# Kernel optimization log

Hardware: AMD Instinct MI355X
Metric: run time of the kernel (lower is better)

## Reference

```python
import jax, jax.numpy as jnp
import numpy as np

N, M, W, F_IN, REP, HYP = 4096, 33, 7, 256, 128, 128
BN_EPS = 1e-5


def setup_inputs() -> dict:
    key = jax.random.key(0)
    ks = iter(jax.random.split(key, 40))
    rn = lambda *s: jax.random.normal(next(ks), s, dtype=jnp.float32) * 0.05
    inp = {
        'X': jax.random.normal(next(ks), (N, M, W, F_IN), dtype=jnp.float32),
        'Y': jax.random.uniform(next(ks), (N, M), dtype=jnp.float32),
        'C': jax.random.uniform(next(ks), (N, M, W), dtype=jnp.float32),
        # message_p.linear
        'msg_W': rn(REP, F_IN), 'msg_b': rn(REP),
        # 2-layer GRU (batch_first) inside message_p
        'gru0_Wih': rn(3 * REP, REP), 'gru0_Whh': rn(3 * REP, REP),
        'gru0_bih': rn(3 * REP), 'gru0_bhh': rn(3 * REP),
        'gru1_Wih': rn(3 * REP, REP), 'gru1_Whh': rn(3 * REP, REP),
        'gru1_bih': rn(3 * REP), 'gru1_bhh': rn(3 * REP),
        # Nei_p.linear (target features -> rep)
        'lin_W': rn(REP, F_IN), 'lin_b': rn(REP),
        # Nei_p.linear2 (2*rep -> rep)
        'lin2_W': rn(REP, 2 * REP), 'lin2_b': rn(REP),
        # GRUCell
        'cell_Wih': rn(3 * REP, REP), 'cell_Whh': rn(3 * REP, REP),
        'cell_bih': rn(3 * REP), 'cell_bhh': rn(3 * REP),
        # hypothesis head
        'hyp_W': rn(HYP, REP), 'hyp_b': rn(HYP),
        'bn_gamma': jnp.ones((HYP,), jnp.float32), 'bn_beta': jnp.zeros((HYP,), jnp.float32),
        'bn_mean': jnp.zeros((HYP,), jnp.float32), 'bn_var': jnp.ones((HYP,), jnp.float32),
        'out_W': rn(1, HYP), 'out_b': rn(1),
    }
    return inp


def _gru_gates(x_gates, h, Whh, bhh):
    # PyTorch GRU/GRUCell math. x_gates = x @ Wih^T + bih, shape [n, 3r]
    hg = h @ Whh.T + bhh
    xr, xz, xn = jnp.split(x_gates, 3, axis=-1)
    hr, hz, hn = jnp.split(hg, 3, axis=-1)
    r = jax.nn.sigmoid(xr + hr)
    z = jax.nn.sigmoid(xz + hz)
    n = jnp.tanh(xn + r * hn)
    return (1.0 - z) * n + z * h


def _gru_layer(x, Wih, Whh, bih, bhh):
    # x: [n, w, d] -> [n, w, r]; scan over time
    xg = jnp.einsum('nwd,gd->nwg', x, Wih) + bih  # [n, w, 3r]
    h0 = jnp.zeros((x.shape[0], Whh.shape[1]), x.dtype)

    def step(h, xg_t):
        h2 = _gru_gates(xg_t, h, Whh, bhh)
        return h2, h2

    _, ys = jax.lax.scan(step, h0, jnp.swapaxes(xg, 0, 1))
    return jnp.swapaxes(ys, 0, 1)


def _forward(X, Y, C, msg_W, msg_b, gru0_Wih, gru0_Whh, gru0_bih, gru0_bhh,
             gru1_Wih, gru1_Whh, gru1_bih, gru1_bhh, lin_W, lin_b, lin2_W, lin2_b,
             cell_Wih, cell_Whh, cell_bih, cell_bhh, hyp_W, hyp_b,
             bn_gamma, bn_beta, bn_mean, bn_var, out_W, out_b):
    target_X = X[:, 0]          # [n, w, f]
    target_Y = Y[:, 0]          # [n]
    neighbor_X = X[:, 1:]       # [n, m-1, w, f]
    neighbor_P = C[:, 1:]       # [n, m-1, w]

    # message_p: linear then weighted sum over neighbors (broadcast-mul-sum)
    h = jnp.einsum('nmwf,rf->nmwr', neighbor_X, msg_W) + msg_b      # [n, m-1, w, r]
    h = jnp.einsum('nmwr,nmw->nwr', h, neighbor_P)                   # [n, w, r]
    h = _gru_layer(h, gru0_Wih, gru0_Whh, gru0_bih, gru0_bhh)
    h_nei = _gru_layer(h, gru1_Wih, gru1_Whh, gru1_bih, gru1_bhh)    # [n, w, r]

    h_self = jnp.einsum('nwf,rf->nwr', target_X, lin_W) + lin_b      # [n, w, r]

    # 7-step cat -> linear2 -> tanh -> GRUCell loop (hx starts at zeros)
    hx0 = jnp.zeros((X.shape[0], lin2_W.shape[0]), X.dtype)

    def step(hx, inputs):
        hn_t, hs_t = inputs
        hx = jnp.tanh(jnp.concatenate((hx, hn_t), axis=-1) @ lin2_W.T + lin2_b)
        xg = hs_t @ cell_Wih.T + cell_bih
        hx = _gru_gates(xg, hx, cell_Whh, cell_bhh)
        return hx, None

    hx, _ = jax.lax.scan(step, hx0, (jnp.swapaxes(h_nei, 0, 1), jnp.swapaxes(h_self, 0, 1)))

    # head: linear -> BN (eval, running stats) -> relu -> linear (dropout = identity)
    h0 = hx @ hyp_W.T + hyp_b
    h0 = (h0 - bn_mean) * jax.lax.rsqrt(bn_var + BN_EPS) * bn_gamma + bn_beta
    h0 = jax.nn.relu(h0)
    y = (h0 @ out_W.T + out_b).reshape(-1)                           # logits [n]

    # binary_cross_entropy_with_logits, mean reduction
    loss = jnp.mean(jnp.maximum(y, 0.0) - y * target_Y + jnp.log1p(jnp.exp(-jnp.abs(y))))
    return loss, jax.nn.sigmoid(y)


def reference(X, Y, C, msg_W, msg_b, gru0_Wih, gru0_Whh, gru0_bih, gru0_bhh,
              gru1_Wih, gru1_Whh, gru1_bih, gru1_bhh, lin_W, lin_b, lin2_W, lin2_b,
              cell_Wih, cell_Whh, cell_bih, cell_bhh, hyp_W, hyp_b,
              bn_gamma, bn_beta, bn_mean, bn_var, out_W, out_b):
    return _forward(X, Y, C, msg_W, msg_b, gru0_Wih, gru0_Whh, gru0_bih, gru0_bhh,
                    gru1_Wih, gru1_Whh, gru1_bih, gru1_bhh, lin_W, lin_b, lin2_W, lin2_b,
                    cell_Wih, cell_Whh, cell_bih, cell_bhh, hyp_W, hyp_b,
                    bn_gamma, bn_beta, bn_mean, bn_var, out_W, out_b)
```

## Files before the change

kernel.cpp:

```cpp
#include <hip/hip_runtime.h>
#include <math.h>

#define N_    4096
#define NPAIR (N_ * 7)

typedef unsigned short u16;
typedef __attribute__((ext_vector_type(8))) short bf16x8;
typedef __attribute__((ext_vector_type(4))) float f32x4;

__device__ __forceinline__ float sigm(float x) { return 1.0f / (1.0f + __expf(-x)); }
__device__ __forceinline__ float tanh_fast(float x) { return 2.0f / (1.0f + __expf(-2.0f * x)) - 1.0f; }
__device__ __forceinline__ float bf2f(u16 u) { return __uint_as_float(((unsigned)u) << 16); }
__device__ __forceinline__ u16 f2bf(float f) {
  unsigned u = __float_as_uint(f);
  return (u16)((u + 0x7FFFu + ((u >> 16) & 1u)) >> 16);
}
__device__ __forceinline__ f32x4 mfma16(bf16x8 a, bf16x8 b, f32x4 c) {
  return __builtin_amdgcn_mfma_f32_16x16x32_bf16(a, b, c, 0, 0, 0);
}

__global__ __launch_bounds__(256) void k_prep_all(
    const float* __restrict__ msg_W, const float* __restrict__ lin_W,
    const float* __restrict__ g0_Wih, const float* __restrict__ g1_Wih,
    const float* __restrict__ c_Wih, const float* __restrict__ lin2_W,
    const float* __restrict__ g0_Whh, const float* __restrict__ g1_Whh,
    const float* __restrict__ c_Whh, const float* __restrict__ hyp_W,
    u16* __restrict__ wbase)
{
  const int task = blockIdx.y;
  const int i = blockIdx.x * 256 + threadIdx.x;
  int R, KD, stride, koff, doff;
  const float* src;
  switch (task) {
    case 0:  R=128; KD=256; stride=256; koff=0;   src=msg_W;  doff=0;      break;
    case 1:  R=128; KD=256; stride=256; koff=0;   src=lin_W;  doff=32768;  break;
    case 2:  R=384; KD=128; stride=128; koff=0;   src=g0_Wih; doff=65536;  break;
    case 3:  R=384; KD=128; stride=128; koff=0;   src=g1_Wih; doff=114688; break;
    case 4:  R=384; KD=128; stride=128; koff=0;   src=c_Wih;  doff=163840; break;
    case 5:  R=128; KD=128; stride=256; koff=128; src=lin2_W; doff=212992; break;
    case 6:  R=128; KD=128; stride=256; koff=0;   src=lin2_W; doff=229376; break;
    case 7:  R=384; KD=128; stride=128; koff=0;   src=g0_Whh; doff=245760; break;
    case 8:  R=384; KD=128; stride=128; koff=0;   src=g1_Whh; doff=294912; break;
    case 9:  R=384; KD=128; stride=128; koff=0;   src=c_Whh;  doff=344064; break;
    default: R=128; KD=128; stride=128; koff=0;   src=hyp_W;  doff=393216; break;
  }
  if (i >= R * KD) return;
  const int r = i / KD, k = i - r * KD;
  wbase[doff + i] = f2bf(src[(size_t)r * stride + koff + k]);
}

__global__ __launch_bounds__(256) void k1_fused(
    const float* __restrict__ X, const float* __restrict__ C,
    const u16* __restrict__ msgw, const u16* __restrict__ linw,
    const float* __restrict__ msg_b, const float* __restrict__ lin_b,
    u16* __restrict__ hmsg, u16* __restrict__ hself)
{
  __shared__ u16 sXW[16 * 256];
  __shared__ u16 sTX[16 * 256];
  __shared__ float s_ps[16];
  const int tid = threadIdx.x, wave = tid >> 6, lane = tid & 63;
  const int p0 = blockIdx.x * 16;

  for (int q = 0; q < 4; ++q) {
    const int lp = wave * 4 + q;
    const int p = p0 + lp;
    const int n = p / 7, w = p - n * 7;
    const float* xb = X + ((size_t)(n * 33 + 1) * 7 + w) * 256 + lane * 4;
    const float* cb = C + (size_t)(n * 33 + 1) * 7 + w;
    float4 acc = make_float4(0.f, 0.f, 0.f, 0.f);
    float ps = 0.f;
    #pragma unroll 4
    for (int m = 0; m < 32; ++m) {
      const float c = cb[m * 7];
      const float4 x4 = *(const float4*)(xb + (size_t)m * 1792);
      acc.x += c * x4.x; acc.y += c * x4.y; acc.z += c * x4.z; acc.w += c * x4.w;
      ps += c;
    }
    const int sb = lp * 512 + ((lane * 8) ^ ((lp & 7) << 4));
    ushort4 o = {f2bf(acc.x), f2bf(acc.y), f2bf(acc.z), f2bf(acc.w)};
    *(ushort4*)((char*)sXW + sb) = o;
    const float4 t4 = *(const float4*)(X + ((size_t)(n * 33) * 7 + w) * 256 + lane * 4);
    ushort4 ot = {f2bf(t4.x), f2bf(t4.y), f2bf(t4.z), f2bf(t4.w)};
    *(ushort4*)((char*)sTX + sb) = ot;
    if (lane == 0) s_ps[lp] = ps;
  }
  __syncthreads();

  const int l15 = lane & 15, lq = lane >> 4;
  bf16x8 ax[8], at[8];
  #pragma unroll
  for (int kc = 0; kc < 8; ++kc) {
    const int off = l15 * 512 + ((lq * 16 + kc * 64) ^ ((l15 & 7) << 4));
    ax[kc] = *(const bf16x8*)((const char*)sXW + off);
    at[kc] = *(const bf16x8*)((const char*)sTX + off);
  }
  float psr[4];
  #pragma unroll
  for (int r = 0; r < 4; ++r) psr[r] = s_ps[lq * 4 + r];

  #pragma unroll
  for (int ct = 0; ct < 2; ++ct) {
    const int col = (wave + ct * 4) * 16 + l15;
    f32x4 am = {0.f, 0.f, 0.f, 0.f}, as = {0.f, 0.f, 0.f, 0.f};
    #pragma unroll
    for (int kc = 0; kc < 8; ++kc) {
      const bf16x8 bm = *(const bf16x8*)(msgw + (size_t)col * 256 + lq * 8 + kc * 32);
      const bf16x8 bl = *(const bf16x8*)(linw + (size_t)col * 256 + lq * 8 + kc * 32);
      am = mfma16(ax[kc], bm, am);
      as = mfma16(at[kc], bl, as);
    }
    const float mb = msg_b[col], lb = lin_b[col];
    #pragma unroll
    for (int r = 0; r < 4; ++r) {
      const int p = p0 + lq * 4 + r;
      hmsg[(size_t)p * 128 + col]  = f2bf(am[r] + mb * psr[r]);
      hself[(size_t)p * 128 + col] = f2bf(as[r] + lb);
    }
  }
}

__device__ __forceinline__ void stage16(u16* __restrict__ dst,
                                        const u16* __restrict__ src,
                                        int n0, int tid)
{
  #pragma unroll
  for (int it = 0; it < 7; ++it) {
    const int chunk = it * 256 + tid;
    const int w = chunk >> 8, rem = chunk & 255;
    const int n = rem >> 4, d0 = (rem & 15) * 8;
    const uint4 v = *(const uint4*)(src + ((size_t)(n0 + n) * 7 + w) * 128 + d0);
    *(uint4*)((char*)dst + w * 4096 + n * 256 + ((d0 * 2) ^ ((n & 7) << 4))) = v;
  }
}

__device__ __forceinline__ void gru_stage(
    u16* __restrict__ sin, u16* __restrict__ sout,
    const u16* __restrict__ wih, const u16* __restrict__ whh,
    const float* __restrict__ bih, const float* __restrict__ bhh,
    int wave, int l15, int lq)
{
  bf16x8 wi[6][4], wh[6][4];
  float binit[6], bxn[2];
  #pragma unroll
  for (int i = 0; i < 6; ++i) {
    const int g = (wave + i * 4) * 16 + l15;
    #pragma unroll
    for (int kc = 0; kc < 4; ++kc) {
      wi[i][kc] = *(const bf16x8*)(wih + (size_t)g * 128 + lq * 8 + kc * 32);
      wh[i][kc] = *(const bf16x8*)(whh + (size_t)g * 128 + lq * 8 + kc * 32);
    }
    binit[i] = (i < 4) ? (bih[g] + bhh[g]) : bhh[g];
    if (i >= 4) bxn[i - 4] = bih[g];
  }
  float hold[2][4] = {{0.f, 0.f, 0.f, 0.f}, {0.f, 0.f, 0.f, 0.f}};

  for (int w = 0; w < 7; ++w) {
    bf16x8 afx[4], afh[4];
    #pragma unroll
    for (int kc = 0; kc < 4; ++kc) {
      const int off = l15 * 256 + ((lq * 16 + kc * 64) ^ ((l15 & 7) << 4));
      afx[kc] = *(const bf16x8*)((const char*)sin + w * 4096 + off);
      if (w) afh[kc] = *(const bf16x8*)((const char*)sout + (w - 1) * 4096 + off);
    }
    f32x4 acc[6], accx[2];
    #pragma unroll
    for (int i = 0; i < 6; ++i) acc[i] = (f32x4){binit[i], binit[i], binit[i], binit[i]};
    #pragma unroll
    for (int t = 0; t < 2; ++t) accx[t] = (f32x4){bxn[t], bxn[t], bxn[t], bxn[t]};

    #pragma unroll
    for (int i = 0; i < 6; ++i) {
      #pragma unroll
      for (int kc = 0; kc < 4; ++kc) {
        if (i < 4) acc[i] = mfma16(afx[kc], wi[i][kc], acc[i]);
        else       accx[i - 4] = mfma16(afx[kc], wi[i][kc], accx[i - 4]);
        if (w) acc[i] = mfma16(afh[kc], wh[i][kc], acc[i]);
      }
    }
    #pragma unroll
    for (int t = 0; t < 2; ++t) {
      const int d = (wave + t * 4) * 16 + l15;
      #pragma unroll
      for (int r = 0; r < 4; ++r) {
        const float rg = sigm(acc[t][r]);
        const float zg = sigm(acc[t + 2][r]);
        const float nn = tanh_fast(accx[t][r] + rg * acc[t + 4][r]);
        const float hv = (1.f - zg) * nn + zg * hold[t][r];
        hold[t][r] = hv;
        const int n = lq * 4 + r;
        *(u16*)((char*)sout + w * 4096 + n * 256 + ((d * 2) ^ ((n & 7) << 4))) = f2bf(hv);
      }
    }
    __syncthreads();
  }
}

__global__ __launch_bounds__(256, 1) void k_chain(
    const u16* __restrict__ hmsg, const u16* __restrict__ hself,
    const u16* __restrict__ wbase,
    const float* __restrict__ g0_bih, const float* __restrict__ g0_bhh,
    const float* __restrict__ g1_bih, const float* __restrict__ g1_bhh,
    const float* __restrict__ lin2_b,
    const float* __restrict__ c_bih, const float* __restrict__ c_bhh,
    const float* __restrict__ hyp_b,
    const float* __restrict__ bn_g, const float* __restrict__ bn_be,
    const float* __restrict__ bn_m, const float* __restrict__ bn_v,
    const float* __restrict__ out_W, const float* __restrict__ out_b,
    const float* __restrict__ Y,
    float* __restrict__ outp, float* __restrict__ bloss)
{
  __shared__ u16 sA[7 * 2048];
  __shared__ u16 sB[7 * 2048];
  __shared__ u16 sC[2048];
  __shared__ u16 sD[2048];
  __shared__ float s_red[16][66];
  __shared__ float s_ls[16];

  const int tid = threadIdx.x;
  const int lane = tid & 63, wave = tid >> 6;
  const int l15 = lane & 15, lq = lane >> 4;
  const int n0 = blockIdx.x * 16;

  const u16* g0wih = wbase + 65536;
  const u16* g1wih = wbase + 114688;
  const u16* cwih  = wbase + 163840;
  const u16* l2w   = wbase + 212992;
  const u16* w2a   = wbase + 229376;
  const u16* whh0  = wbase + 245760;
  const u16* whh1  = wbase + 294912;
  const u16* whhc  = wbase + 344064;
  const u16* hypw  = wbase + 393216;

  stage16(sA, hmsg, n0, tid);
  __syncthreads();

  gru_stage(sA, sB, g0wih, whh0, g0_bih, g0_bhh, wave, l15, lq);
  gru_stage(sB, sA, g1wih, whh1, g1_bih, g1_bhh, wave, l15, lq);

  stage16(sB, hself, n0, tid);
  __syncthreads();

  {
    bf16x8 lw[2][4], wa[2][4], wi[6][4], wh[6][4];
    float b2[2], cbin[6], cbxn[2];
    #pragma unroll
    for (int t = 0; t < 2; ++t) {
      const int d = (wave + t * 4) * 16 + l15;
      #pragma unroll
      for (int kc = 0; kc < 4; ++kc) {
        lw[t][kc] = *(const bf16x8*)(l2w + (size_t)d * 128 + lq * 8 + kc * 32);
        wa[t][kc] = *(const bf16x8*)(w2a + (size_t)d * 128 + lq * 8 + kc * 32);
      }
      b2[t] = lin2_b[d];
    }
    #pragma unroll
    for (int i = 0; i < 6; ++i) {
      const int g = (wave + i * 4) * 16 + l15;
      #pragma unroll
      for (int kc = 0; kc < 4; ++kc) {
        wi[i][kc] = *(const bf16x8*)(cwih + (size_t)g * 128 + lq * 8 + kc * 32);
        wh[i][kc] = *(const bf16x8*)(whhc + (size_t)g * 128 + lq * 8 + kc * 32);
      }
      cbin[i] = (i < 4) ? (c_bih[g] + c_bhh[g]) : c_bhh[g];
      if (i >= 4) cbxn[i - 4] = c_bih[g];
    }

    for (int w = 0; w < 7; ++w) {
      bf16x8 af1[4], afx_[4];
      #pragma unroll
      for (int kc = 0; kc < 4; ++kc) {
        const int off = l15 * 256 + ((lq * 16 + kc * 64) ^ ((l15 & 7) << 4));
        af1[kc] = *(const bf16x8*)((const char*)sA + w * 4096 + off);
        if (w) afx_[kc] = *(const bf16x8*)((const char*)sD + off);
      }
      f32x4 a1[2];
      #pragma unroll
      for (int t = 0; t < 2; ++t) a1[t] = (f32x4){b2[t], b2[t], b2[t], b2[t]};
      #pragma unroll
      for (int t = 0; t < 2; ++t)
        #pragma unroll
        for (int kc = 0; kc < 4; ++kc) {
          a1[t] = mfma16(af1[kc], lw[t][kc], a1[t]);
          if (w) a1[t] = mfma16(afx_[kc], wa[t][kc], a1[t]);
        }
      float hx1[2][4];
      #pragma unroll
      for (int t = 0; t < 2; ++t) {
        const int d = (wave + t * 4) * 16 + l15;
        #pragma unroll
        for (int r = 0; r < 4; ++r) {
          hx1[t][r] = tanh_fast(a1[t][r]);
          const int n = lq * 4 + r;
          *(u16*)((char*)sC + n * 256 + ((d * 2) ^ ((n & 7) << 4))) = f2bf(hx1[t][r]);
        }
      }
      __syncthreads();

      bf16x8 afs[4], aft[4];
      #pragma unroll
      for (int kc = 0; kc < 4; ++kc) {
        const int off = l15 * 256 + ((lq * 16 + kc * 64) ^ ((l15 & 7) << 4));
        afs[kc] = *(const bf16x8*)((const char*)sB + w * 4096 + off);
        aft[kc] = *(const bf16x8*)((const char*)sC + off);
      }
      f32x4 acc[6], accx[2];
      #pragma unroll
      for (int i = 0; i < 6; ++i) acc[i] = (f32x4){cbin[i], cbin[i], cbin[i], cbin[i]};
      #pragma unroll
      for (int t = 0; t < 2; ++t) accx[t] = (f32x4){cbxn[t], cbxn[t], cbxn[t], cbxn[t]};
      #pragma unroll
      for (int i = 0; i < 6; ++i)
        #pragma unroll
        for (int kc = 0; kc < 4; ++kc) {
          if (i < 4) acc[i] = mfma16(afs[kc], wi[i][kc], acc[i]);
          else       accx[i - 4] = mfma16(afs[kc], wi[i][kc], accx[i - 4]);
          acc[i] = mfma16(aft[kc], wh[i][kc], acc[i]);
        }
      #pragma unroll
      for (int t = 0; t < 2; ++t) {
        const int d = (wave + t * 4) * 16 + l15;
        #pragma unroll
        for (int r = 0; r < 4; ++r) {
          const float rg = sigm(acc[t][r]);
          const float zg = sigm(acc[t + 2][r]);
          const float nn = tanh_fast(accx[t][r] + rg * acc[t + 4][r]);
          const float hv = (1.f - zg) * nn + zg * hx1[t][r];
          const int n = lq * 4 + r;
          *(u16*)((char*)sD + n * 256 + ((d * 2) ^ ((n & 7) << 4))) = f2bf(hv);
        }
      }
      __syncthreads();
    }
  }

  {
    bf16x8 af[4];
    #pragma unroll
    for (int kc = 0; kc < 4; ++kc) {
      const int off = l15 * 256 + ((lq * 16 + kc * 64) ^ ((l15 & 7) << 4));
      af[kc] = *(const bf16x8*)((const char*)sD + off);
    }
    f32x4 ah[2];
    float sc[2], mu[2], be[2], ow[2];
    #pragma unroll
    for (int t = 0; t < 2; ++t) {
      const int q = (wave + t * 4) * 16 + l15;
      const float hb = hyp_b[q];
      ah[t] = (f32x4){hb, hb, hb, hb};
      sc[t] = rsqrtf(bn_v[q] + 1e-5f) * bn_g[q];
      mu[t] = bn_m[q]; be[t] = bn_be[q]; ow[t] = out_W[q];
      #pragma unroll
      for (int kc = 0; kc < 4; ++kc) {
        const bf16x8 hf = *(const bf16x8*)(hypw + (size_t)q * 128 + lq * 8 + kc * 32);
        ah[t] = mfma16(af[kc], hf, ah[t]);
      }
    }
    float part[4] = {0.f, 0.f, 0.f, 0.f};
    #pragma unroll
    for (int t = 0; t < 2; ++t)
      #pragma unroll
      for (int r = 0; r < 4; ++r) {
        const float v = (ah[t][r] - mu[t]) * sc[t] + be[t];
        part[r] += ow[t] * fmaxf(v, 0.f);
      }
    #pragma unroll
    for (int r = 0; r < 4; ++r) s_red[lq * 4 + r][wave * 16 + l15] = part[r];
  }
  __syncthreads();
  if (tid < 16) {
    const int n = tid;
    float y = out_b[0];
    #pragma unroll 8
    for (int c = 0; c < 64; ++c) y += s_red[n][c];
    outp[1 + n0 + n] = 1.f / (1.f + __expf(-y));
    const float tY = Y[(size_t)(n0 + n) * 33];
    s_ls[n] = fmaxf(y, 0.f) - y * tY + log1pf(__expf(-fabsf(y)));
  }
  __syncthreads();
  if (tid == 0) {
    float s = 0.f;
    #pragma unroll
    for (int j = 0; j < 16; ++j) s += s_ls[j];
    bloss[blockIdx.x] = s;
  }
}

__global__ __launch_bounds__(256) void k3_loss(const float* __restrict__ bloss,
                                               float* __restrict__ out)
{
  __shared__ float s[256];
  s[threadIdx.x] = bloss[threadIdx.x];
  __syncthreads();
  for (int off = 128; off > 0; off >>= 1) {
    if (threadIdx.x < off) s[threadIdx.x] += s[threadIdx.x + off];
    __syncthreads();
  }
  if (threadIdx.x == 0) out[0] = s[0] * (1.0f / 4096.0f);
}

extern "C" void kernel_launch(void* const* d_in, const int* in_sizes, int n_in,
                              void* d_out, int out_size, void* d_ws, size_t ws_size,
                              hipStream_t stream) {
  const float* X       = (const float*)d_in[0];
  const float* Y       = (const float*)d_in[1];
  const float* C       = (const float*)d_in[2];
  const float* msg_W   = (const float*)d_in[3];
  const float* msg_b   = (const float*)d_in[4];
  const float* g0_Wih  = (const float*)d_in[5];
  const float* g0_Whh  = (const float*)d_in[6];
  const float* g0_bih  = (const float*)d_in[7];
  const float* g0_bhh  = (const float*)d_in[8];
  const float* g1_Wih  = (const float*)d_in[9];
  const float* g1_Whh  = (const float*)d_in[10];
  const float* g1_bih  = (const float*)d_in[11];
  const float* g1_bhh  = (const float*)d_in[12];
  const float* lin_W   = (const float*)d_in[13];
  const float* lin_b   = (const float*)d_in[14];
  const float* lin2_W  = (const float*)d_in[15];
  const float* lin2_b  = (const float*)d_in[16];
  const float* c_Wih   = (const float*)d_in[17];
  const float* c_Whh   = (const float*)d_in[18];
  const float* c_bih   = (const float*)d_in[19];
  const float* c_bhh   = (const float*)d_in[20];
  const float* hyp_W   = (const float*)d_in[21];
  const float* hyp_b   = (const float*)d_in[22];
  const float* bn_g    = (const float*)d_in[23];
  const float* bn_be   = (const float*)d_in[24];
  const float* bn_m    = (const float*)d_in[25];
  const float* bn_v    = (const float*)d_in[26];
  const float* out_W   = (const float*)d_in[27];
  const float* out_b   = (const float*)d_in[28];

  const size_t P = NPAIR;
  u16* hmsg  = (u16*)d_ws;
  u16* hself = hmsg  + P * 128;
  u16* wbase = hself + P * 128;
  float* bloss = (float*)(wbase + 409600);

  float* out = (float*)d_out;

  k_prep_all<<<dim3(192, 11), 256, 0, stream>>>(msg_W, lin_W, g0_Wih, g1_Wih,
      c_Wih, lin2_W, g0_Whh, g1_Whh, c_Whh, hyp_W, wbase);

  k1_fused<<<NPAIR / 16, 256, 0, stream>>>(X, C, wbase, wbase + 32768,
      msg_b, lin_b, hmsg, hself);

  k_chain<<<N_ / 16, 256, 0, stream>>>(hmsg, hself, wbase,
      g0_bih, g0_bhh, g1_bih, g1_bhh, lin2_b, c_bih, c_bhh,
      hyp_b, bn_g, bn_be, bn_m, bn_v, out_W, out_b, Y, out, bloss);

  k3_loss<<<1, 256, 0, stream>>>(bloss, out);
}
```

Before: 252.2 us.

## Remap k1 to one block per node with contiguous slab loads

Reorganises the neighbor-weighted reduction so each block handles one node's full contiguous X slab (33x7x256). Waves split the 32 neighbors, and partial sums are reduced in shared memory instead of each wave striding through memory for a single (n,w) pair. C is staged in shared memory and the per-w C sums are computed once. The 16-row MFMA tile is now only 7/16 occupied, so part of the MFMA work and output rows are wasted. In exchange, global X reads become fully contiguous and more loads are in flight.

```diff
diff --git a/kernel.cpp b/kernel.cpp
--- a/kernel.cpp
+++ b/kernel.cpp
@@ -55,34 +55,68 @@
     const float* __restrict__ msg_b, const float* __restrict__ lin_b,
     u16* __restrict__ hmsg, u16* __restrict__ hself)
 {
+  __shared__ float s_part[4][7][260];
   __shared__ u16 sXW[16 * 256];
   __shared__ u16 sTX[16 * 256];
-  __shared__ float s_ps[16];
-  const int tid = threadIdx.x, wave = tid >> 6, lane = tid & 63;
-  const int p0 = blockIdx.x * 16;
-
-  for (int q = 0; q < 4; ++q) {
-    const int lp = wave * 4 + q;
-    const int p = p0 + lp;
-    const int n = p / 7, w = p - n * 7;
-    const float* xb = X + ((size_t)(n * 33 + 1) * 7 + w) * 256 + lane * 4;
-    const float* cb = C + (size_t)(n * 33 + 1) * 7 + w;
-    float4 acc = make_float4(0.f, 0.f, 0.f, 0.f);
-    float ps = 0.f;
-    #pragma unroll 4
-    for (int m = 0; m < 32; ++m) {
-      const float c = cb[m * 7];
-      const float4 x4 = *(const float4*)(xb + (size_t)m * 1792);
-      acc.x += c * x4.x; acc.y += c * x4.y; acc.z += c * x4.z; acc.w += c * x4.w;
-      ps += c;
-    }
-    const int sb = lp * 512 + ((lane * 8) ^ ((lp & 7) << 4));
-    ushort4 o = {f2bf(acc.x), f2bf(acc.y), f2bf(acc.z), f2bf(acc.w)};
-    *(ushort4*)((char*)sXW + sb) = o;
-    const float4 t4 = *(const float4*)(X + ((size_t)(n * 33) * 7 + w) * 256 + lane * 4);
-    ushort4 ot = {f2bf(t4.x), f2bf(t4.y), f2bf(t4.z), f2bf(t4.w)};
-    *(ushort4*)((char*)sTX + sb) = ot;
-    if (lane == 0) s_ps[lp] = ps;
+  __shared__ float s_c[224];
+  __shared__ float s_ps[8];
+  const int tid = threadIdx.x, lane = tid & 63, wave = tid >> 6;
+  const int n = blockIdx.x;
+  const size_t slab = (size_t)n * 59136;
+
+  {
+    uint4 z = {0, 0, 0, 0};
+    *(uint4*)&sXW[tid * 8] = z;
+    *(uint4*)&sXW[2048 + tid * 8] = z;
+    *(uint4*)&sTX[tid * 8] = z;
+    *(uint4*)&sTX[2048 + tid * 8] = z;
+  }
+  if (tid < 224) s_c[tid] = C[(size_t)n * 231 + 7 + tid];
+  __syncthreads();
+
+  if (tid < 7) {
+    float s = 0.f;
+    #pragma unroll 8
+    for (int j = 0; j < 32; ++j) s += s_c[j * 7 + tid];
+    s_ps[tid] = s;
+  }
+
+  float4 acc[7];
+  #pragma unroll
+  for (int w = 0; w < 7; ++w) acc[w] = make_float4(0.f, 0.f, 0.f, 0.f);
+  {
+    const float* xr0 = X + slab + (size_t)(1 + wave * 8) * 1792 + lane * 4;
+    #pragma unroll 2
+    for (int mi = 0; mi < 8; ++mi) {
+      const int m = wave * 8 + mi;
+      const float* xr = xr0 + (size_t)mi * 1792;
+      #pragma unroll
+      for (int w = 0; w < 7; ++w) {
+        const float c = s_c[m * 7 + w];
+        const float4 x4 = *(const float4*)(xr + w * 256);
+        acc[w].x += c * x4.x; acc[w].y += c * x4.y;
+        acc[w].z += c * x4.z; acc[w].w += c * x4.w;
+      }
+    }
+  }
+  #pragma unroll
+  for (int w = 0; w < 7; ++w)
+    *(float4*)&s_part[wave][w][lane * 4] = acc[w];
+
+  #pragma unroll
+  for (int it = 0; it < 7; ++it) {
+    const int i = it * 256 + tid;
+    const int w = i >> 8, f = i & 255;
+    const float v = X[slab + (size_t)w * 256 + f];
+    *(u16*)((char*)sTX + w * 512 + ((f * 2) ^ ((w & 7) << 4))) = f2bf(v);
+  }
+  __syncthreads();
+
+  #pragma unroll
+  for (int w = 0; w < 7; ++w) {
+    const float v = s_part[0][w][tid] + s_part[1][w][tid] +
+                    s_part[2][w][tid] + s_part[3][w][tid];
+    *(u16*)((char*)sXW + w * 512 + ((tid * 2) ^ ((w & 7) << 4))) = f2bf(v);
   }
   __syncthreads();
 
@@ -94,10 +128,6 @@
     ax[kc] = *(const bf16x8*)((const char*)sXW + off);
     at[kc] = *(const bf16x8*)((const char*)sTX + off);
   }
-  float psr[4];
-  #pragma unroll
-  for (int r = 0; r < 4; ++r) psr[r] = s_ps[lq * 4 + r];
-
   #pragma unroll
   for (int ct = 0; ct < 2; ++ct) {
     const int col = (wave + ct * 4) * 16 + l15;
@@ -112,9 +142,12 @@
     const float mb = msg_b[col], lb = lin_b[col];
     #pragma unroll
     for (int r = 0; r < 4; ++r) {
-      const int p = p0 + lq * 4 + r;
-      hmsg[(size_t)p * 128 + col]  = f2bf(am[r] + mb * psr[r]);
-      hself[(size_t)p * 128 + col] = f2bf(as[r] + lb);
+      const int row = lq * 4 + r;
+      if (row < 7) {
+        const int p = n * 7 + row;
+        hmsg[(size_t)p * 128 + col]  = f2bf(am[r] + mb * s_ps[row]);
+        hself[(size_t)p * 128 + col] = f2bf(as[r] + lb);
+      }
     }
   }
 }
@@ -442,7 +475,7 @@
   k_prep_all<<<dim3(192, 11), 256, 0, stream>>>(msg_W, lin_W, g0_Wih, g1_Wih,
       c_Wih, lin2_W, g0_Whh, g1_Whh, c_Whh, hyp_W, wbase);
 
-  k1_fused<<<NPAIR / 16, 256, 0, stream>>>(X, C, wbase, wbase + 32768,
+  k1_fused<<<N_, 256, 0, stream>>>(X, C, wbase, wbase + 32768,
       msg_b, lin_b, hmsg, hself);
 
   k_chain<<<N_ / 16, 256, 0, stream>>>(hmsg, hself, wbase,
```

Result: slower. 269.1 us (+6.7%).

## Use 8 waves per chain block, stage C in LDS, nontemporal X loads

Applied to the files above, without the earlier changes.

The recurrent chain kernel now runs 512 threads per block, so each wave owns one 16-column slice of the hidden dimension instead of two. This halves per-thread weight registers and targets two blocks per CU for more latency hiding in the serial GRU steps. In the first kernel, the C coefficients for a block are preloaded into shared memory and X is streamed with nontemporal loads. The cost is more waves joining each barrier and a larger reduction buffer.

```diff
diff --git a/kernel.cpp b/kernel.cpp
--- a/kernel.cpp
+++ b/kernel.cpp
@@ -57,30 +57,39 @@
 {
   __shared__ u16 sXW[16 * 256];
   __shared__ u16 sTX[16 * 256];
+  __shared__ float s_c[4][224];
   __shared__ float s_ps[16];
   const int tid = threadIdx.x, wave = tid >> 6, lane = tid & 63;
   const int p0 = blockIdx.x * 16;
+  const int nfirst = p0 / 7;
+
+  for (int i = tid; i < 896; i += 256) {
+    const int nn = nfirst + i / 224;
+    s_c[i / 224][i % 224] = (nn < N_) ? C[(size_t)nn * 231 + 7 + (i % 224)] : 0.f;
+  }
+  __syncthreads();
 
   for (int q = 0; q < 4; ++q) {
     const int lp = wave * 4 + q;
     const int p = p0 + lp;
     const int n = p / 7, w = p - n * 7;
-    const float* xb = X + ((size_t)(n * 33 + 1) * 7 + w) * 256 + lane * 4;
-    const float* cb = C + (size_t)(n * 33 + 1) * 7 + w;
-    float4 acc = make_float4(0.f, 0.f, 0.f, 0.f);
+    const float* cr = &s_c[n - nfirst][0];
+    const f32x4* xb = (const f32x4*)(X + ((size_t)(n * 33 + 1) * 7 + w) * 256) + lane;
+    f32x4 acc = {0.f, 0.f, 0.f, 0.f};
     float ps = 0.f;
-    #pragma unroll 4
+    #pragma unroll 8
     for (int m = 0; m < 32; ++m) {
-      const float c = cb[m * 7];
-      const float4 x4 = *(const float4*)(xb + (size_t)m * 1792);
-      acc.x += c * x4.x; acc.y += c * x4.y; acc.z += c * x4.z; acc.w += c * x4.w;
+      const float c = cr[m * 7 + w];
+      const f32x4 x4 = __builtin_nontemporal_load(xb + (size_t)m * 448);
+      acc += x4 * c;
       ps += c;
     }
     const int sb = lp * 512 + ((lane * 8) ^ ((lp & 7) << 4));
-    ushort4 o = {f2bf(acc.x), f2bf(acc.y), f2bf(acc.z), f2bf(acc.w)};
+    ushort4 o = {f2bf(acc[0]), f2bf(acc[1]), f2bf(acc[2]), f2bf(acc[3])};
     *(ushort4*)((char*)sXW + sb) = o;
-    const float4 t4 = *(const float4*)(X + ((size_t)(n * 33) * 7 + w) * 256 + lane * 4);
-    ushort4 ot = {f2bf(t4.x), f2bf(t4.y), f2bf(t4.z), f2bf(t4.w)};
+    const f32x4 t4 = __builtin_nontemporal_load(
+        (const f32x4*)(X + ((size_t)n * 231 + w) * 256) + lane);
+    ushort4 ot = {f2bf(t4[0]), f2bf(t4[1]), f2bf(t4[2]), f2bf(t4[3])};
     *(ushort4*)((char*)sTX + sb) = ot;
     if (lane == 0) s_ps[lp] = ps;
   }
@@ -123,36 +132,34 @@
                                         const u16* __restrict__ src,
                                         int n0, int tid)
 {
-  #pragma unroll
-  for (int it = 0; it < 7; ++it) {
-    const int chunk = it * 256 + tid;
-    const int w = chunk >> 8, rem = chunk & 255;
+  for (int i = tid; i < 1792; i += 512) {
+    const int w = i >> 8, rem = i & 255;
     const int n = rem >> 4, d0 = (rem & 15) * 8;
     const uint4 v = *(const uint4*)(src + ((size_t)(n0 + n) * 7 + w) * 128 + d0);
     *(uint4*)((char*)dst + w * 4096 + n * 256 + ((d0 * 2) ^ ((n & 7) << 4))) = v;
   }
 }
 
-__device__ __forceinline__ void gru_stage(
-    u16* __restrict__ sin, u16* __restrict__ sout,
+__device__ __forceinline__ void gru_stage8(
+    const u16* __restrict__ sin, u16* __restrict__ sout,
     const u16* __restrict__ wih, const u16* __restrict__ whh,
     const float* __restrict__ bih, const float* __restrict__ bhh,
-    int wave, int l15, int lq)
-{
-  bf16x8 wi[6][4], wh[6][4];
-  float binit[6], bxn[2];
+    int d, int l15, int lq)
+{
+  bf16x8 wiR[4], wiZ[4], wiN[4], whR[4], whZ[4], whN[4];
   #pragma unroll
-  for (int i = 0; i < 6; ++i) {
-    const int g = (wave + i * 4) * 16 + l15;
-    #pragma unroll
-    for (int kc = 0; kc < 4; ++kc) {
-      wi[i][kc] = *(const bf16x8*)(wih + (size_t)g * 128 + lq * 8 + kc * 32);
-      wh[i][kc] = *(const bf16x8*)(whh + (size_t)g * 128 + lq * 8 + kc * 32);
-    }
-    binit[i] = (i < 4) ? (bih[g] + bhh[g]) : bhh[g];
-    if (i >= 4) bxn[i - 4] = bih[g];
-  }
-  float hold[2][4] = {{0.f, 0.f, 0.f, 0.f}, {0.f, 0.f, 0.f, 0.f}};
+  for (int kc = 0; kc < 4; ++kc) {
+    wiR[kc] = *(const bf16x8*)(wih + (size_t)d * 128 + lq * 8 + kc * 32);
+    wiZ[kc] = *(const bf16x8*)(wih + (size_t)(d + 128) * 128 + lq * 8 + kc * 32);
+    wiN[kc] = *(const bf16x8*)(wih + (size_t)(d + 256) * 128 + lq * 8 + kc * 32);
+    whR[kc] = *(const bf16x8*)(whh + (size_t)d * 128 + lq * 8 + kc * 32);
+    whZ[kc] = *(const bf16x8*)(whh + (size_t)(d + 128) * 128 + lq * 8 + kc * 32);
+    whN[kc] = *(const bf16x8*)(whh + (size_t)(d + 256) * 128 + lq * 8 + kc * 32);
+  }
+  const float bR = bih[d] + bhh[d];
+  const float bZ = bih[d + 128] + bhh[d + 128];
+  const float bNh = bhh[d + 256], bNx = bih[d + 256];
+  float hold[4] = {0.f, 0.f, 0.f, 0.f};
 
   for (int w = 0; w < 7; ++w) {
     bf16x8 afx[4], afh[4];
@@ -162,40 +169,34 @@
       afx[kc] = *(const bf16x8*)((const char*)sin + w * 4096 + off);
       if (w) afh[kc] = *(const bf16x8*)((const char*)sout + (w - 1) * 4096 + off);
     }
-    f32x4 acc[6], accx[2];
-    #pragma unroll
-    for (int i = 0; i < 6; ++i) acc[i] = (f32x4){binit[i], binit[i], binit[i], binit[i]};
-    #pragma unroll
-    for (int t = 0; t < 2; ++t) accx[t] = (f32x4){bxn[t], bxn[t], bxn[t], bxn[t]};
-
-    #pragma unroll
-    for (int i = 0; i < 6; ++i) {
-      #pragma unroll
-      for (int kc = 0; kc < 4; ++kc) {
-        if (i < 4) acc[i] = mfma16(afx[kc], wi[i][kc], acc[i]);
-        else       accx[i - 4] = mfma16(afx[kc], wi[i][kc], accx[i - 4]);
-        if (w) acc[i] = mfma16(afh[kc], wh[i][kc], acc[i]);
-      }
-    }
-    #pragma unroll
-    for (int t = 0; t < 2; ++t) {
-      const int d = (wave + t * 4) * 16 + l15;
-      #pragma unroll
-      for (int r = 0; r < 4; ++r) {
-        const float rg = sigm(acc[t][r]);
-        const float zg = sigm(acc[t + 2][r]);
-        const float nn = tanh_fast(accx[t][r] + rg * acc[t + 4][r]);
-        const float hv = (1.f - zg) * nn + zg * hold[t][r];
-        hold[t][r] = hv;
-        const int n = lq * 4 + r;
-        *(u16*)((char*)sout + w * 4096 + n * 256 + ((d * 2) ^ ((n & 7) << 4))) = f2bf(hv);
-      }
+    f32x4 aR = {bR, bR, bR, bR}, aZ = {bZ, bZ, bZ, bZ};
+    f32x4 aNh = {bNh, bNh, bNh, bNh}, aNx = {bNx, bNx, bNx, bNx};
+    #pragma unroll
+    for (int kc = 0; kc < 4; ++kc) {
+      aR  = mfma16(afx[kc], wiR[kc], aR);
+      aZ  = mfma16(afx[kc], wiZ[kc], aZ);
+      aNx = mfma16(afx[kc], wiN[kc], aNx);
+      if (w) {
+        aR  = mfma16(afh[kc], whR[kc], aR);
+        aZ  = mfma16(afh[kc], whZ[kc], aZ);
+        aNh = mfma16(afh[kc], whN[kc], aNh);
+      }
+    }
+    #pragma unroll
+    for (int r = 0; r < 4; ++r) {
+      const float rg = sigm(aR[r]);
+      const float zg = sigm(aZ[r]);
+      const float nn = tanh_fast(aNx[r] + rg * aNh[r]);
+      const float hv = (1.f - zg) * nn + zg * hold[r];
+      hold[r] = hv;
+      const int n = lq * 4 + r;
+      *(u16*)((char*)sout + w * 4096 + n * 256 + ((d * 2) ^ ((n & 7) << 4))) = f2bf(hv);
     }
     __syncthreads();
   }
 }
 
-__global__ __launch_bounds__(256, 1) void k_chain(
+__global__ __launch_bounds__(512, 2) void k_chain(
     const u16* __restrict__ hmsg, const u16* __restrict__ hself,
     const u16* __restrict__ wbase,
     const float* __restrict__ g0_bih, const float* __restrict__ g0_bhh,
@@ -213,12 +214,13 @@
   __shared__ u16 sB[7 * 2048];
   __shared__ u16 sC[2048];
   __shared__ u16 sD[2048];
-  __shared__ float s_red[16][66];
+  __shared__ float s_red[16][130];
   __shared__ float s_ls[16];
 
   const int tid = threadIdx.x;
   const int lane = tid & 63, wave = tid >> 6;
   const int l15 = lane & 15, lq = lane >> 4;
+  const int d = wave * 16 + l15;
   const int n0 = blockIdx.x * 16;
 
   const u16* g0wih = wbase + 65536;
@@ -234,36 +236,29 @@
   stage16(sA, hmsg, n0, tid);
   __syncthreads();
 
-  gru_stage(sA, sB, g0wih, whh0, g0_bih, g0_bhh, wave, l15, lq);
-  gru_stage(sB, sA, g1wih, whh1, g1_bih, g1_bhh, wave, l15, lq);
+  gru_stage8(sA, sB, g0wih, whh0, g0_bih, g0_bhh, d, l15, lq);
+  gru_stage8(sB, sA, g1wih, whh1, g1_bih, g1_bhh, d, l15, lq);
 
   stage16(sB, hself, n0, tid);
   __syncthreads();
 
   {
-    bf16x8 lw[2][4], wa[2][4], wi[6][4], wh[6][4];
-    float b2[2], cbin[6], cbxn[2];
-    #pragma unroll
-    for (int t = 0; t < 2; ++t) {
-      const int d = (wave + t * 4) * 16 + l15;
-      #pragma unroll
-      for (int kc = 0; kc < 4; ++kc) {
-        lw[t][kc] = *(const bf16x8*)(l2w + (size_t)d * 128 + lq * 8 + kc * 32);
-        wa[t][kc] = *(const bf16x8*)(w2a + (size_t)d * 128 + lq * 8 + kc * 32);
-      }
-      b2[t] = lin2_b[d];
-    }
-    #pragma unroll
-    for (int i = 0; i < 6; ++i) {
-      const int g = (wave + i * 4) * 16 + l15;
-      #pragma unroll
-      for (int kc = 0; kc < 4; ++kc) {
-        wi[i][kc] = *(const bf16x8*)(cwih + (size_t)g * 128 + lq * 8 + kc * 32);
-        wh[i][kc] = *(const bf16x8*)(whhc + (size_t)g * 128 + lq * 8 + kc * 32);
-      }
-      cbin[i] = (i < 4) ? (c_bih[g] + c_bhh[g]) : c_bhh[g];
-      if (i >= 4) cbxn[i - 4] = c_bih[g];
-    }
+    bf16x8 lw[4], wa[4], wiR[4], wiZ[4], wiN[4], whR[4], whZ[4], whN[4];
+    #pragma unroll
+    for (int kc = 0; kc < 4; ++kc) {
+      lw[kc]  = *(const bf16x8*)(l2w + (size_t)d * 128 + lq * 8 + kc * 32);
+      wa[kc]  = *(const bf16x8*)(w2a + (size_t)d * 128 + lq * 8 + kc * 32);
+      wiR[kc] = *(const bf16x8*)(cwih + (size_t)d * 128 + lq * 8 + kc * 32);
+      wiZ[kc] = *(const bf16x8*)(cwih + (size_t)(d + 128) * 128 + lq * 8 + kc * 32);
+      wiN[kc] = *(const bf16x8*)(cwih + (size_t)(d + 256) * 128 + lq * 8 + kc * 32);
+      whR[kc] = *(const bf16x8*)(whhc + (size_t)d * 128 + lq * 8 + kc * 32);
+      whZ[kc] = *(const bf16x8*)(whhc + (size_t)(d + 128) * 128 + lq * 8 + kc * 32);
+      whN[kc] = *(const bf16x8*)(whhc + (size_t)(d + 256) * 128 + lq * 8 + kc * 32);
+    }
+    const float b2 = lin2_b[d];
+    const float bR = c_bih[d] + c_bhh[d];
+    const float bZ = c_bih[d + 128] + c_bhh[d + 128];
+    const float bNh = c_bhh[d + 256], bNx = c_bih[d + 256];
 
     for (int w = 0; w < 7; ++w) {
       bf16x8 af1[4], afx_[4];
@@ -273,26 +268,18 @@
         af1[kc] = *(const bf16x8*)((const char*)sA + w * 4096 + off);
         if (w) afx_[kc] = *(const bf16x8*)((const char*)sD + off);
       }
-      f32x4 a1[2];
-      #pragma unroll
-      for (int t = 0; t < 2; ++t) a1[t] = (f32x4){b2[t], b2[t], b2[t], b2[t]};
-      #pragma unroll
-      for (int t = 0; t < 2; ++t)
-        #pragma unroll
-        for (int kc = 0; kc < 4; ++kc) {
-          a1[t] = mfma16(af1[kc], lw[t][kc], a1[t]);
-          if (w) a1[t] = mfma16(afx_[kc], wa[t][kc], a1[t]);
-        }
-      float hx1[2][4];
-      #pragma unroll
-      for (int t = 0; t < 2; ++t) {
-        const int d = (wave + t * 4) * 16 + l15;
-        #pragma unroll
-        for (int r = 0; r < 4; ++r) {
-          hx1[t][r] = tanh_fast(a1[t][r]);
-          const int n = lq * 4 + r;
-          *(u16*)((char*)sC + n * 256 + ((d * 2) ^ ((n & 7) << 4))) = f2bf(hx1[t][r]);
-        }
+      f32x4 a1 = {b2, b2, b2, b2};
+      #pragma unroll
+      for (int kc = 0; kc < 4; ++kc) {
+        a1 = mfma16(af1[kc], lw[kc], a1);
+        if (w) a1 = mfma16(afx_[kc], wa[kc], a1);
+      }
+      float hx1[4];
+      #pragma unroll
+      for (int r = 0; r < 4; ++r) {
+        hx1[r] = tanh_fast(a1[r]);
+        const int n = lq * 4 + r;
+        *(u16*)((char*)sC + n * 256 + ((d * 2) ^ ((n & 7) << 4))) = f2bf(hx1[r]);
       }
       __syncthreads();
 
@@ -303,31 +290,25 @@
         afs[kc] = *(const bf16x8*)((const char*)sB + w * 4096 + off);
         aft[kc] = *(const bf16x8*)((const char*)sC + off);
       }
-      f32x4 acc[6], accx[2];
-      #pragma unroll
-      for (int i = 0; i < 6; ++i) acc[i] = (f32x4){cbin[i], cbin[i], cbin[i], cbin[i]};
-      #pragma unroll
-      for (int t = 0; t < 2; ++t) accx[t] = (f32x4){cbxn[t], cbxn[t], cbxn[t], cbxn[t]};
-      #pragma unroll
-      for (int i = 0; i < 6; ++i)
-        #pragma unroll
-        for (int kc = 0; kc < 4; ++kc) {
-          if (i < 4) acc[i] = mfma16(afs[kc], wi[i][kc], acc[i]);
-          else       accx[i - 4] = mfma16(afs[kc], wi[i][kc], accx[i - 4]);
-          acc[i] = mfma16(aft[kc], wh[i][kc], acc[i]);
-        }
-      #pragma unroll
-      for (int t = 0; t < 2; ++t) {
-        const int d = (wave + t * 4) * 16 + l15;
-        #pragma unroll
-        for (int r = 0; r < 4; ++r) {
-          const float rg = sigm(acc[t][r]);
-          const float zg = sigm(acc[t + 2][r]);
-          const float nn = tanh_fast(accx[t][r] + rg * acc[t + 4][r]);
-          const float hv = (1.f - zg) * nn + zg * hx1[t][r];
-          const int n = lq * 4 + r;
-          *(u16*)((char*)sD + n * 256 + ((d * 2) ^ ((n & 7) << 4))) = f2bf(hv);
-        }
+      f32x4 aR = {bR, bR, bR, bR}, aZ = {bZ, bZ, bZ, bZ};
+      f32x4 aNh = {bNh, bNh, bNh, bNh}, aNx = {bNx, bNx, bNx, bNx};
+      #pragma unroll
+      for (int kc = 0; kc < 4; ++kc) {
+        aR  = mfma16(afs[kc], wiR[kc], aR);
+        aZ  = mfma16(afs[kc], wiZ[kc], aZ);
+        aNx = mfma16(afs[kc], wiN[kc], aNx);
+        aR  = mfma16(aft[kc], whR[kc], aR);
+        aZ  = mfma16(aft[kc], whZ[kc], aZ);
+        aNh = mfma16(aft[kc], whN[kc], aNh);
+      }
+      #pragma unroll
+      for (int r = 0; r < 4; ++r) {
+        const float rg = sigm(aR[r]);
+        const float zg = sigm(aZ[r]);
+        const float nn = tanh_fast(aNx[r] + rg * aNh[r]);
+        const float hv = (1.f - zg) * nn + zg * hx1[r];
+        const int n = lq * 4 + r;
+        *(u16*)((char*)sD + n * 256 + ((d * 2) ^ ((n & 7) << 4))) = f2bf(hv);
       }
       __syncthreads();
     }
@@ -340,38 +321,27 @@
       const int off = l15 * 256 + ((lq * 16 + kc * 64) ^ ((l15 & 7) << 4));
       af[kc] = *(const bf16x8*)((const char*)sD + off);
     }
-    f32x4 ah[2];
-    float sc[2], mu[2], be[2], ow[2];
-    #pragma unroll
-    for (int t = 0; t < 2; ++t) {
-      const int q = (wave + t * 4) * 16 + l15;
-      const float hb = hyp_b[q];
-      ah[t] = (f32x4){hb, hb, hb, hb};
-      sc[t] = rsqrtf(bn_v[q] + 1e-5f) * bn_g[q];
-      mu[t] = bn_m[q]; be[t] = bn_be[q]; ow[t] = out_W[q];
-      #pragma unroll
-      for (int kc = 0; kc < 4; ++kc) {
-        const bf16x8 hf = *(const bf16x8*)(hypw + (size_t)q * 128 + lq * 8 + kc * 32);
-        ah[t] = mfma16(af[kc], hf, ah[t]);
-      }
-    }
-    float part[4] = {0.f, 0.f, 0.f, 0.f};
-    #pragma unroll
-    for (int t = 0; t < 2; ++t)
-      #pragma unroll
-      for (int r = 0; r < 4; ++r) {
-        const float v = (ah[t][r] - mu[t]) * sc[t] + be[t];
-        part[r] += ow[t] * fmaxf(v, 0.f);
-      }
-    #pragma unroll
-    for (int r = 0; r < 4; ++r) s_red[lq * 4 + r][wave * 16 + l15] = part[r];
+    const float hb = hyp_b[d];
+    f32x4 ah = {hb, hb, hb, hb};
+    #pragma unroll
+    for (int kc = 0; kc < 4; ++kc) {
+      const bf16x8 hf = *(const bf16x8*)(hypw + (size_t)d * 128 + lq * 8 + kc * 32);
+      ah = mfma16(af[kc], hf, ah);
+    }
+    const float sc = rsqrtf(bn_v[d] + 1e-5f) * bn_g[d];
+    const float mu = bn_m[d], be = bn_be[d], ow = out_W[d];
+    #pragma unroll
+    for (int r = 0; r < 4; ++r) {
+      const float v = (ah[r] - mu) * sc + be;
+      s_red[lq * 4 + r][d] = ow * fmaxf(v, 0.f);
+    }
   }
   __syncthreads();
   if (tid < 16) {
     const int n = tid;
     float y = out_b[0];
     #pragma unroll 8
-    for (int c = 0; c < 64; ++c) y += s_red[n][c];
+    for (int c = 0; c < 128; ++c) y += s_red[n][c];
     outp[1 + n0 + n] = 1.f / (1.f + __expf(-y));
     const float tY = Y[(size_t)(n0 + n) * 33];
     s_ls[n] = fmaxf(y, 0.f) - y * tY + log1pf(__expf(-fabsf(y)));
@@ -445,7 +415,7 @@
   k1_fused<<<NPAIR / 16, 256, 0, stream>>>(X, C, wbase, wbase + 32768,
       msg_b, lin_b, hmsg, hself);
 
-  k_chain<<<N_ / 16, 256, 0, stream>>>(hmsg, hself, wbase,
+  k_chain<<<N_ / 16, 512, 0, stream>>>(hmsg, hself, wbase,
       g0_bih, g0_bhh, g1_bih, g1_bhh, lin2_b, c_bih, c_bhh,
       hyp_b, bn_g, bn_be, bn_m, bn_v, out_W, out_b, Y, out, bloss);
 
```

Result: faster. 233.2 us (median of 2 runs) (-7.5%).
